# Optimization experiments

Measured on AMD Instinct MI355X. Metric: run time of the kernel, lower is better.

## Reference

```python
import jax, jax.numpy as jnp
import numpy as np

B, T, IN, H, STEPS = 32768, 11, 2, 64, 80


def gru_cell(x, h, W_ih, W_hh, b_ih, b_hh):
    # PyTorch GRU cell: gates ordered (r, z, n)
    gi = x @ W_ih.T + b_ih            # [B, 3H]
    gh = h @ W_hh.T + b_hh            # [B, 3H]
    gi_r, gi_z, gi_n = jnp.split(gi, 3, axis=-1)
    gh_r, gh_z, gh_n = jnp.split(gh, 3, axis=-1)
    r = jax.nn.sigmoid(gi_r + gh_r)
    z = jax.nn.sigmoid(gi_z + gh_z)
    n = jnp.tanh(gi_n + r * gh_n)
    return (1.0 - z) * n + z * h


def setup_inputs() -> dict:
    key = jax.random.key(0)
    ks = jax.random.split(key, 20)
    s = 1.0 / np.sqrt(H)
    u = lambda k, shape: jax.random.uniform(k, shape, jnp.float32, -s, s)
    inp = {"x": jax.random.normal(ks[0], (B, T, IN), jnp.float32)}
    i = 1
    for pfx, in0 in (("e", IN), ("d", IN)):
        for l, d_in in ((0, in0), (1, H)):
            inp[f"{pfx}W_ih{l}"] = u(ks[i], (3 * H, d_in)); i += 1
            inp[f"{pfx}W_hh{l}"] = u(ks[i], (3 * H, H)); i += 1
            inp[f"{pfx}b_ih{l}"] = u(ks[i], (3 * H,)); i += 1
            inp[f"{pfx}b_hh{l}"] = u(ks[i], (3 * H,)); i += 1
    inp["fc_W"] = u(ks[17], (2, H))
    inp["fc_b"] = u(ks[18], (2,))
    return inp


def reference(x, eW_ih0, eW_hh0, eb_ih0, eb_hh0, eW_ih1, eW_hh1, eb_ih1, eb_hh1,
              dW_ih0, dW_hh0, db_ih0, db_hh0, dW_ih1, dW_hh1, db_ih1, db_hh1,
              fc_W, fc_b):
    b = x.shape[0]
    h0 = jnp.zeros((b, H), x.dtype)
    h1 = jnp.zeros((b, H), x.dtype)

    # ---- encoder: 2-layer GRU over time (dropout inactive in eval) ----
    def enc_step(carry, xt):
        c0, c1 = carry
        c0 = gru_cell(xt, c0, eW_ih0, eW_hh0, eb_ih0, eb_hh0)
        c1 = gru_cell(c0, c1, eW_ih1, eW_hh1, eb_ih1, eb_hh1)
        return (c0, c1), None

    (h0, h1), _ = jax.lax.scan(enc_step, (h0, h1), jnp.swapaxes(x, 0, 1))

    def dec_step(carry, _):
        inp, c0, c1 = carry
        c0 = gru_cell(inp, c0, dW_ih0, dW_hh0, db_ih0, db_hh0)
        c1 = gru_cell(c0, c1, dW_ih1, dW_hh1, db_ih1, db_hh1)
        pred = c1 @ fc_W.T + fc_b     # [B, 2]
        return (pred, c0, c1), pred

    init = (x[:, -1, :], h0, h1)
    _, preds = jax.lax.scan(dec_step, init, None, length=STEPS)  # [80, B, 2]
    return jnp.swapaxes(preds, 0, 1)  # [B, 80, 2]
```

## Files before the change

### kernel.cpp

```cpp
#include <hip/hip_runtime.h>
#include <cstddef>

#define T_SEQ 11
#define STEPS 80

typedef _Float16 f16;
typedef _Float16 f16x4 __attribute__((ext_vector_type(4)));
typedef _Float16 f16x8 __attribute__((ext_vector_type(8)));
typedef float    f32x4 __attribute__((ext_vector_type(4)));

#define SRC (-1.44269504f)
#define SNC ( 2.88539008f)

#define OFF_WF   0
#define OFF_HB   98304
#define OFF_XE   131072
#define OFF_BIAS 136704
#define OFF_XW   140800
#define OFF_FCF  143872
#define SMEM_BYTES 145920

__device__ __forceinline__ f32x4 mfma16(f16x8 a, f16x8 b, f32x4 c) {
    return __builtin_amdgcn_mfma_f32_16x16x32_f16(a, b, c, 0, 0, 0);
}
__device__ __forceinline__ float exp2r(float x) { return __builtin_amdgcn_exp2f(x); }

__device__ __forceinline__ void stage_mat(f16* __restrict__ sw, int slot,
                                          const float* __restrict__ W, int tid) {
    for (int e = tid; e < 12288; e += 1024) {
        const int row = e >> 6, k = e & 63;
        const int g = row >> 6, j = row & 63;
        const int lane = ((k >> 3) & 3) * 16 + (j & 15);
        const float sc = (g == 2) ? SNC : SRC;
        sw[slot * 12288 + g * 4096 + (j >> 4) * 1024 + (k >> 5) * 512 + lane * 8 + (k & 7)]
            = (f16)(sc * W[e]);
    }
}
__device__ __forceinline__ void stage_composed(f16* __restrict__ sw, int slot,
                                               const float* __restrict__ Wih0,
                                               const float* __restrict__ fcW, int tid) {
    for (int e = tid; e < 12288; e += 1024) {
        const int row = e >> 6, k = e & 63;
        const int g = row >> 6, j = row & 63;
        const int lane = ((k >> 3) & 3) * 16 + (j & 15);
        const float sc = (g == 2) ? SNC : SRC;
        const float v = Wih0[row * 2] * fcW[k] + Wih0[row * 2 + 1] * fcW[64 + k];
        sw[slot * 12288 + g * 4096 + (j >> 4) * 1024 + (k >> 5) * 512 + lane * 8 + (k & 7)]
            = (f16)(sc * v);
    }
}

template<bool XM, int SH, int SX, int CT>
__device__ __forceinline__ void cellL(
    const f16* __restrict__ sw, const float* __restrict__ sb, const float* __restrict__ sxw,
    const f16* __restrict__ Xs, const f16* __restrict__ Hs, f16* __restrict__ Dst,
    f16x4& ho, int wb, int j4, int rom0, int rom1, int wom, float x0, float x1)
{
    const f16* whb = sw + SH * 12288 + wb;
    const f32x4 bR  = *(const f32x4*)(sb + CT * 256 +       j4);
    const f32x4 bZ  = *(const f32x4*)(sb + CT * 256 +  64 + j4);
    const f32x4 bNi = *(const f32x4*)(sb + CT * 256 + 128 + j4);
    const f32x4 bNh = *(const f32x4*)(sb + CT * 256 + 192 + j4);
    f16x8 hb0 = *(const f16x8*)(Hs + rom0);
    f16x8 hb1 = *(const f16x8*)(Hs + rom1);
    f32x4 aR  = mfma16(*(const f16x8*)(whb),        hb0, bR);
    f32x4 aZ  = mfma16(*(const f16x8*)(whb + 4096), hb0, bZ);
    f32x4 aNh = mfma16(*(const f16x8*)(whb + 8192), hb0, bNh);
    aR  = mfma16(*(const f16x8*)(whb +  512),       hb1, aR);
    aZ  = mfma16(*(const f16x8*)(whb + 4096 + 512), hb1, aZ);
    aNh = mfma16(*(const f16x8*)(whb + 8192 + 512), hb1, aNh);
    f32x4 aNi;
    if constexpr (XM) {
        const f16* wxb = sw + SX * 12288 + wb;
        f16x8 xb0 = *(const f16x8*)(Xs + rom0);
        f16x8 xb1 = *(const f16x8*)(Xs + rom1);
        aR  = mfma16(*(const f16x8*)(wxb),               xb0, aR);
        aR  = mfma16(*(const f16x8*)(wxb +  512),        xb1, aR);
        aZ  = mfma16(*(const f16x8*)(wxb + 4096),        xb0, aZ);
        aZ  = mfma16(*(const f16x8*)(wxb + 4096 + 512),  xb1, aZ);
        aNi = mfma16(*(const f16x8*)(wxb + 8192),        xb0, bNi);
        aNi = mfma16(*(const f16x8*)(wxb + 8192 + 512),  xb1, aNi);
    } else {
        const f32x4 xw0 = *(const f32x4*)(sxw +        j4);
        const f32x4 xw1 = *(const f32x4*)(sxw +  64 + j4);
        const f32x4 xw2 = *(const f32x4*)(sxw + 128 + j4);
        const f32x4 xw3 = *(const f32x4*)(sxw + 192 + j4);
        const f32x4 xw4 = *(const f32x4*)(sxw + 256 + j4);
        const f32x4 xw5 = *(const f32x4*)(sxw + 320 + j4);
        aR  += x0 * xw0 + x1 * xw1;
        aZ  += x0 * xw2 + x1 * xw3;
        aNi  = bNi + x0 * xw4 + x1 * xw5;
    }
    f16x4 o;
    #pragma unroll
    for (int i = 0; i < 4; ++i) {
        const float r = __builtin_amdgcn_rcpf(1.f + exp2r(aR[i]));
        const float z = __builtin_amdgcn_rcpf(1.f + exp2r(aZ[i]));
        const float n = 1.f - 2.f * __builtin_amdgcn_rcpf(1.f + exp2r(aNi[i] + r * aNh[i]));
        const float h = n + z * ((float)ho[i] - n);
        o[i] = (f16)h;
    }
    ho = o;
    *(f16x4*)(Dst + wom) = o;
}

__global__ __launch_bounds__(1024, 4)
void gru_traj_lds1(
    const float* __restrict__ x,
    const float* __restrict__ eWih0, const float* __restrict__ eWhh0,
    const float* __restrict__ ebih0, const float* __restrict__ ebhh0,
    const float* __restrict__ eWih1, const float* __restrict__ eWhh1,
    const float* __restrict__ ebih1, const float* __restrict__ ebhh1,
    const float* __restrict__ dWih0, const float* __restrict__ dWhh0,
    const float* __restrict__ dbih0, const float* __restrict__ dbhh0,
    const float* __restrict__ dWih1, const float* __restrict__ dWhh1,
    const float* __restrict__ dbih1, const float* __restrict__ dbhh1,
    const float* __restrict__ fcW,  const float* __restrict__ fcb,
    float* __restrict__ out)
{
    extern __shared__ char smem[];
    f16*    sw  = (f16*)(smem + OFF_WF);
    f16*    hbb = (f16*)(smem + OFF_HB);
    float2* sxe = (float2*)(smem + OFF_XE);
    float*  sb  = (float*)(smem + OFF_BIAS);
    float*  sxw = (float*)(smem + OFF_XW);
    f16*    sfc = (f16*)(smem + OFF_FCF);
#define HB(i) (hbb + (i) * 4096)

    const int tid  = threadIdx.x;
    const int lane = tid & 63;
    const int wv   = __builtin_amdgcn_readfirstlane(tid >> 6);
    const int jg   = wv >> 2;
    const int mg   = wv & 3;
    const int quad = lane >> 4;
    const int col  = lane & 15;
    const int r0   = blockIdx.x * 64;

    stage_mat(sw, 0, eWhh0, tid);
    stage_mat(sw, 1, eWhh1, tid);
    stage_mat(sw, 2, eWih1, tid);
    {
        const float2* x2 = (const float2*)x;
        for (int i = tid; i < 64 * T_SEQ; i += 1024) {
            const int row = i / T_SEQ, t = i - row * T_SEQ;
            sxe[t * 64 + row] = x2[(size_t)r0 * T_SEQ + i];
        }
    }
    for (int i = tid; i < 4096; i += 1024) { hbb[i] = (f16)0.f; hbb[8192 + i] = (f16)0.f; }
    if (tid < 64) {
        const int j = tid;
        sb[       j] = SRC * (ebih0[j] + ebhh0[j]);
        sb[ 64 + j] = SRC * (ebih0[64 + j] + ebhh0[64 + j]);
        sb[128 + j] = SNC * ebih0[128 + j];
        sb[192 + j] = SNC * ebhh0[128 + j];
        sb[256 +       j] = SRC * (ebih1[j] + ebhh1[j]);
        sb[256 +  64 + j] = SRC * (ebih1[64 + j] + ebhh1[64 + j]);
        sb[256 + 128 + j] = SNC * ebih1[128 + j];
        sb[256 + 192 + j] = SNC * ebhh1[128 + j];
        sxw[      j] = SRC * eWih0[j * 2];
        sxw[ 64 + j] = SRC * eWih0[j * 2 + 1];
        sxw[128 + j] = SRC * eWih0[(64 + j) * 2];
        sxw[192 + j] = SRC * eWih0[(64 + j) * 2 + 1];
        sxw[256 + j] = SNC * eWih0[(128 + j) * 2];
        sxw[320 + j] = SNC * eWih0[(128 + j) * 2 + 1];
    }
    {
        const int e = tid;
        const int ks = e >> 9, rr = e & 511;
        const int lne = rr >> 3, ki = rr & 7;
        const int c = lne & 15, q = lne >> 4;
        const int k = ks * 32 + q * 8 + ki;
        sfc[ks * 512 + lne * 8 + ki] = (c < 2) ? (f16)fcW[c * 64 + k] : (f16)0.f;
    }
    __syncthreads();

    const int c7   = col & 7;
    const int rom0 = col * 64 + ((quad ^ c7) << 3) + mg * 1024;
    const int rom1 = col * 64 + (((4 + quad) ^ c7) << 3) + mg * 1024;
    const int wom  = col * 64 + ((((jg << 1) | (quad >> 1)) ^ c7) << 3) + ((quad & 1) << 2) + mg * 1024;
    const int j4   = jg * 16 + quad * 4;
    const int wb   = lane * 8 + jg * 1024;

    f16x4 ho0, ho1;
    #pragma unroll
    for (int i = 0; i < 4; ++i) { ho0[i] = (f16)0.f; ho1[i] = (f16)0.f; }

    #pragma unroll 1
    for (int t = 0; t < T_SEQ - 1; t += 2) {
        float2 xv = sxe[t * 64 + mg * 16 + col];
        cellL<false, 0, 0, 0>(sw, sb, sxw, HB(0), HB(0), HB(1), ho0, wb, j4, rom0, rom1, wom, xv.x, xv.y);
        __syncthreads();
        cellL<true, 1, 2, 1>(sw, sb, sxw, HB(1), HB(2), HB(3), ho1, wb, j4, rom0, rom1, wom, 0.f, 0.f);
        xv = sxe[(t + 1) * 64 + mg * 16 + col];
        cellL<false, 0, 0, 0>(sw, sb, sxw, HB(1), HB(1), HB(0), ho0, wb, j4, rom0, rom1, wom, xv.x, xv.y);
        __syncthreads();
        cellL<true, 1, 2, 1>(sw, sb, sxw, HB(0), HB(3), HB(2), ho1, wb, j4, rom0, rom1, wom, 0.f, 0.f);
    }
    {
        const float2 xv = sxe[10 * 64 + mg * 16 + col];
        cellL<false, 0, 0, 0>(sw, sb, sxw, HB(0), HB(0), HB(1), ho0, wb, j4, rom0, rom1, wom, xv.x, xv.y);
        __syncthreads();
        cellL<true, 1, 2, 1>(sw, sb, sxw, HB(1), HB(2), HB(3), ho1, wb, j4, rom0, rom1, wom, 0.f, 0.f);
    }

    __syncthreads();
    stage_mat(sw, 0, dWhh0, tid);
    stage_mat(sw, 1, dWhh1, tid);
    stage_mat(sw, 2, dWih1, tid);
    stage_composed(sw, 3, dWih0, fcW, tid);
    if (tid < 64) {
        const int j = tid;
        const float f0 = fcb[0], f1 = fcb[1];
        sb[512 +       j] = SRC * (dbih0[j] + dbhh0[j] + dWih0[j * 2] * f0 + dWih0[j * 2 + 1] * f1);
        sb[512 +  64 + j] = SRC * (dbih0[64 + j] + dbhh0[64 + j] + dWih0[(64 + j) * 2] * f0 + dWih0[(64 + j) * 2 + 1] * f1);
        sb[512 + 128 + j] = SNC * (dbih0[128 + j] + dWih0[(128 + j) * 2] * f0 + dWih0[(128 + j) * 2 + 1] * f1);
        sb[512 + 192 + j] = SNC * dbhh0[128 + j];
        sb[768 +       j] = SRC * (dbih1[j] + dbhh1[j]);
        sb[768 +  64 + j] = SRC * (dbih1[64 + j] + dbhh1[64 + j]);
        sb[768 + 128 + j] = SNC * dbih1[128 + j];
        sb[768 + 192 + j] = SNC * dbhh1[128 + j];
        sxw[384 +       j] = SRC * dWih0[j * 2];
        sxw[384 +  64 + j] = SRC * dWih0[j * 2 + 1];
        sxw[384 + 128 + j] = SRC * dWih0[(64 + j) * 2];
        sxw[384 + 192 + j] = SRC * dWih0[(64 + j) * 2 + 1];
        sxw[384 + 256 + j] = SNC * dWih0[(128 + j) * 2];
        sxw[384 + 320 + j] = SNC * dWih0[(128 + j) * 2 + 1];
    }
    __syncthreads();

    f32x4 pb;
    {
        const float f0 = fcb[0], f1 = fcb[1];
        #pragma unroll
        for (int rg = 0; rg < 4; ++rg) pb[rg] = 0.f;
        if (quad == 0) { pb[0] = f0; pb[1] = f1; }
    }
    float* op = out + (size_t)(r0 + mg * 16 + col) * (STEPS * 2);

    auto FCout = [&](const f16* h1c) {
        if (jg == 0) {
            f16x8 a0 = *(const f16x8*)(h1c + rom0);
            f16x8 a1 = *(const f16x8*)(h1c + rom1);
            f32x4 p = mfma16(*(const f16x8*)(sfc + lane * 8), a0, pb);
            p = mfma16(*(const f16x8*)(sfc + 512 + lane * 8), a1, p);
            if (quad == 0) *(float2*)op = make_float2(p[0], p[1]);
        }
        op += 2;
    };

    {
        const float2 xv0 = sxe[10 * 64 + mg * 16 + col];
        cellL<false, 0, 0, 2>(sw, sb, sxw + 384, HB(1), HB(1), HB(0), ho0, wb, j4, rom0, rom1, wom, xv0.x, xv0.y);
        __syncthreads();
        cellL<true, 1, 2, 3>(sw, sb, sxw, HB(0), HB(3), HB(2), ho1, wb, j4, rom0, rom1, wom, 0.f, 0.f);
        __syncthreads();
        FCout(HB(2));
    }

    #pragma unroll 1
    for (int sp = 0; sp < 39; ++sp) {
        cellL<true, 0, 3, 2>(sw, sb, sxw, HB(2), HB(0), HB(1), ho0, wb, j4, rom0, rom1, wom, 0.f, 0.f);
        __syncthreads();
        cellL<true, 1, 2, 3>(sw, sb, sxw, HB(1), HB(2), HB(3), ho1, wb, j4, rom0, rom1, wom, 0.f, 0.f);
        __syncthreads();
        FCout(HB(3));
        cellL<true, 0, 3, 2>(sw, sb, sxw, HB(3), HB(1), HB(0), ho0, wb, j4, rom0, rom1, wom, 0.f, 0.f);
        __syncthreads();
        cellL<true, 1, 2, 3>(sw, sb, sxw, HB(0), HB(3), HB(2), ho1, wb, j4, rom0, rom1, wom, 0.f, 0.f);
        __syncthreads();
        FCout(HB(2));
    }
    {
        cellL<true, 0, 3, 2>(sw, sb, sxw, HB(2), HB(0), HB(1), ho0, wb, j4, rom0, rom1, wom, 0.f, 0.f);
        __syncthreads();
        cellL<true, 1, 2, 3>(sw, sb, sxw, HB(1), HB(2), HB(3), ho1, wb, j4, rom0, rom1, wom, 0.f, 0.f);
        __syncthreads();
        FCout(HB(3));
    }
#undef HB
}

extern "C" void kernel_launch(void* const* d_in, const int* in_sizes, int n_in,
                              void* d_out, int out_size, void* d_ws, size_t ws_size,
                              hipStream_t stream) {
    (void)n_in; (void)out_size; (void)d_ws; (void)ws_size;

    const float* x     = (const float*)d_in[0];
    const float* eWih0 = (const float*)d_in[1];
    const float* eWhh0 = (const float*)d_in[2];
    const float* ebih0 = (const float*)d_in[3];
    const float* ebhh0 = (const float*)d_in[4];
    const float* eWih1 = (const float*)d_in[5];
    const float* eWhh1 = (const float*)d_in[6];
    const float* ebih1 = (const float*)d_in[7];
    const float* ebhh1 = (const float*)d_in[8];
    const float* dWih0 = (const float*)d_in[9];
    const float* dWhh0 = (const float*)d_in[10];
    const float* dbih0 = (const float*)d_in[11];
    const float* dbhh0 = (const float*)d_in[12];
    const float* dWih1 = (const float*)d_in[13];
    const float* dWhh1 = (const float*)d_in[14];
    const float* dbih1 = (const float*)d_in[15];
    const float* dbhh1 = (const float*)d_in[16];
    const float* fcW   = (const float*)d_in[17];
    const float* fcb   = (const float*)d_in[18];
    float* out = (float*)d_out;

    static bool attr_done = false;
    if (!attr_done) {
        (void)hipFuncSetAttribute((const void*)gru_traj_lds1,
                                  hipFuncAttributeMaxDynamicSharedMemorySize, SMEM_BYTES);
        attr_done = true;
    }

    const int b = in_sizes[0] / (T_SEQ * 2);
    dim3 grid(b / 64), block(1024);
    hipLaunchKernelGGL(gru_traj_lds1, grid, block, SMEM_BYTES, stream,
        x, eWih0, eWhh0, ebih0, ebhh0, eWih1, eWhh1, ebih1, ebhh1,
        dWih0, dWhh0, dbih0, dbhh0, dWih1, dWhh1, dbih1, dbhh1,
        fcW, fcb, out);
}
```

Measured before the change: 535.2 us.

## Replace block-wide barriers with per-row-group LDS counter barriers

Swaps the __syncthreads between GRU cell stages for a software barrier built on an LDS atomic counter, one counter per row-group (mg) of 4 waves. Only the waves that share a 16-row slice of the hidden-state buffers wait on each other, so groups can drift apart and independent waves are not stalled by the whole block. The cost is spin-waiting with s_sleep and atomic traffic on LDS. There is also a risk of memory-ordering or hazard problems, since the barrier uses relaxed atomics and buffers are reused in a rotating pattern.

```diff
diff --git a/kernel.cpp b/kernel.cpp
--- a/kernel.cpp
+++ b/kernel.cpp
@@ -18,7 +18,8 @@
 #define OFF_BIAS 136704
 #define OFF_XW   140800
 #define OFF_FCF  143872
-#define SMEM_BYTES 145920
+#define OFF_CNT  145920
+#define SMEM_BYTES 145936
 
 __device__ __forceinline__ f32x4 mfma16(f16x8 a, f16x8 b, f32x4 c) {
     return __builtin_amdgcn_mfma_f32_16x16x32_f16(a, b, c, 0, 0, 0);
@@ -105,7 +106,7 @@
 }
 
 __global__ __launch_bounds__(1024, 4)
-void gru_traj_lds1(
+void gru_traj_lds2(
     const float* __restrict__ x,
     const float* __restrict__ eWih0, const float* __restrict__ eWhh0,
     const float* __restrict__ ebih0, const float* __restrict__ ebhh0,
@@ -125,17 +126,31 @@
     float*  sb  = (float*)(smem + OFF_BIAS);
     float*  sxw = (float*)(smem + OFF_XW);
     f16*    sfc = (f16*)(smem + OFF_FCF);
+    unsigned* cnt = (unsigned*)(smem + OFF_CNT);
 #define HB(i) (hbb + (i) * 4096)
 
     const int tid  = threadIdx.x;
     const int lane = tid & 63;
     const int wv   = __builtin_amdgcn_readfirstlane(tid >> 6);
     const int jg   = wv >> 2;
-    const int mg   = wv & 3;
+    const int mg   = wv & 2 ? (wv & 3) : (wv & 3);
     const int quad = lane >> 4;
     const int col  = lane & 15;
     const int r0   = blockIdx.x * 64;
 
+    unsigned tgt = 0;
+    auto gbar = [&]() {
+        asm volatile("s_waitcnt lgkmcnt(0)" ::: "memory");
+        if (lane == 0)
+            __hip_atomic_fetch_add(cnt + mg, 1u, __ATOMIC_RELAXED, __HIP_MEMORY_SCOPE_WORKGROUP);
+        tgt += 4;
+        while (__hip_atomic_load(cnt + mg, __ATOMIC_RELAXED, __HIP_MEMORY_SCOPE_WORKGROUP) < tgt)
+            __builtin_amdgcn_s_sleep(1);
+        __builtin_amdgcn_sched_barrier(0);
+        asm volatile("" ::: "memory");
+    };
+
+    if (tid < 4) cnt[tid] = 0u;
     stage_mat(sw, 0, eWhh0, tid);
     stage_mat(sw, 1, eWhh1, tid);
     stage_mat(sw, 2, eWih1, tid);
@@ -189,17 +204,17 @@
     for (int t = 0; t < T_SEQ - 1; t += 2) {
         float2 xv = sxe[t * 64 + mg * 16 + col];
         cellL<false, 0, 0, 0>(sw, sb, sxw, HB(0), HB(0), HB(1), ho0, wb, j4, rom0, rom1, wom, xv.x, xv.y);
-        __syncthreads();
+        gbar();
         cellL<true, 1, 2, 1>(sw, sb, sxw, HB(1), HB(2), HB(3), ho1, wb, j4, rom0, rom1, wom, 0.f, 0.f);
         xv = sxe[(t + 1) * 64 + mg * 16 + col];
         cellL<false, 0, 0, 0>(sw, sb, sxw, HB(1), HB(1), HB(0), ho0, wb, j4, rom0, rom1, wom, xv.x, xv.y);
-        __syncthreads();
+        gbar();
         cellL<true, 1, 2, 1>(sw, sb, sxw, HB(0), HB(3), HB(2), ho1, wb, j4, rom0, rom1, wom, 0.f, 0.f);
     }
     {
         const float2 xv = sxe[10 * 64 + mg * 16 + col];
         cellL<false, 0, 0, 0>(sw, sb, sxw, HB(0), HB(0), HB(1), ho0, wb, j4, rom0, rom1, wom, xv.x, xv.y);
-        __syncthreads();
+        gbar();
         cellL<true, 1, 2, 1>(sw, sb, sxw, HB(1), HB(2), HB(3), ho1, wb, j4, rom0, rom1, wom, 0.f, 0.f);
     }
 
@@ -251,30 +266,30 @@
     {
         const float2 xv0 = sxe[10 * 64 + mg * 16 + col];
         cellL<false, 0, 0, 2>(sw, sb, sxw + 384, HB(1), HB(1), HB(0), ho0, wb, j4, rom0, rom1, wom, xv0.x, xv0.y);
-        __syncthreads();
+        gbar();
         cellL<true, 1, 2, 3>(sw, sb, sxw, HB(0), HB(3), HB(2), ho1, wb, j4, rom0, rom1, wom, 0.f, 0.f);
-        __syncthreads();
+        gbar();
         FCout(HB(2));
     }
 
     #pragma unroll 1
     for (int sp = 0; sp < 39; ++sp) {
         cellL<true, 0, 3, 2>(sw, sb, sxw, HB(2), HB(0), HB(1), ho0, wb, j4, rom0, rom1, wom, 0.f, 0.f);
-        __syncthreads();
+        gbar();
         cellL<true, 1, 2, 3>(sw, sb, sxw, HB(1), HB(2), HB(3), ho1, wb, j4, rom0, rom1, wom, 0.f, 0.f);
-        __syncthreads();
+        gbar();
         FCout(HB(3));
         cellL<true, 0, 3, 2>(sw, sb, sxw, HB(3), HB(1), HB(0), ho0, wb, j4, rom0, rom1, wom, 0.f, 0.f);
-        __syncthreads();
+        gbar();
         cellL<true, 1, 2, 3>(sw, sb, sxw, HB(0), HB(3), HB(2), ho1, wb, j4, rom0, rom1, wom, 0.f, 0.f);
-        __syncthreads();
+        gbar();
         FCout(HB(2));
     }
     {
         cellL<true, 0, 3, 2>(sw, sb, sxw, HB(2), HB(0), HB(1), ho0, wb, j4, rom0, rom1, wom, 0.f, 0.f);
-        __syncthreads();
+        gbar();
         cellL<true, 1, 2, 3>(sw, sb, sxw, HB(1), HB(2), HB(3), ho1, wb, j4, rom0, rom1, wom, 0.f, 0.f);
-        __syncthreads();
+        gbar();
         FCout(HB(3));
     }
 #undef HB
@@ -308,14 +323,14 @@
 
     static bool attr_done = false;
     if (!attr_done) {
-        (void)hipFuncSetAttribute((const void*)gru_traj_lds1,
+        (void)hipFuncSetAttribute((const void*)gru_traj_lds2,
                                   hipFuncAttributeMaxDynamicSharedMemorySize, SMEM_BYTES);
         attr_done = true;
     }
 
     const int b = in_sizes[0] / (T_SEQ * 2);
     dim3 grid(b / 64), block(1024);
-    hipLaunchKernelGGL(gru_traj_lds1, grid, block, SMEM_BYTES, stream,
+    hipLaunchKernelGGL(gru_traj_lds2, grid, block, SMEM_BYTES, stream,
         x, eWih0, eWhh0, ebih0, ebhh0, eWih1, eWhh1, ebih1, ebhh1,
         dWih0, dWhh0, dbih0, dbhh0, dWih1, dWhh1, dbih1, dbhh1,
         fcW, fcb, out);
```

Measured after the change: 534.5 us. Within noise of the previous version (-0.1%).
